# Performance work log

Measured on AMD Instinct MI355X. Metric: run time of the kernel, lower is better.

Reference implementation:

```python
import jax, jax.numpy as jnp
import numpy as np

LUT_DIM = 33  # standard 33^3 color LUT


def setup_inputs() -> dict:
    key = jax.random.key(0)
    k1, k2 = jax.random.split(key)
    # learned 3D LUT: [out_channels=3, D_b, D_g, D_r]
    lut = jax.random.normal(k1, (3, LUT_DIM, LUT_DIM, LUT_DIM), dtype=jnp.float32) * 0.1
    # input image batch in [0, 1): [B, 3, H, W]
    x = jax.random.uniform(k2, (4, 3, 1024, 1024), dtype=jnp.float32)
    return {"lut": lut, "x": x}


def reference(lut, x):
    """Trilinear interpolation of a 3D color LUT (image-adaptive-3DLUT forward).

    lut: [3, D, D, D] laid out as lut[c, ib, ig, ir] (flat index ir + ig*D + ib*D*D)
    x:   [B, 3, H, W] with channels (r, g, b) in [0, 1]
    returns: [B, 3, H, W]
    """
    dim = lut.shape[-1]
    scale = dim - 1  # 1 / binsize

    r, g, b = x[:, 0], x[:, 1], x[:, 2]  # each [B, H, W]

    def cell(c):
        s = c * scale
        idx = jnp.clip(jnp.floor(s), 0, scale - 1).astype(jnp.int32)
        return idx, s - idx.astype(s.dtype)  # integer cell, fractional offset

    ir, dr = cell(r)
    ig, dg = cell(g)
    ib, db = cell(b)

    lut_flat = lut.reshape(3, -1)  # [3, D^3], tiny and cache-resident

    out = jnp.zeros((3,) + r.shape, dtype=x.dtype)  # [3, B, H, W]
    # 8 corners of the enclosing LUT cell, trilinear weights
    for or_ in (0, 1):
        wr = dr if or_ else (1.0 - dr)
        for og in (0, 1):
            wg = dg if og else (1.0 - dg)
            for ob in (0, 1):
                wb = db if ob else (1.0 - db)
                flat = ((ib + ob) * dim + (ig + og)) * dim + (ir + or_)  # [B, H, W]
                corner = lut_flat[:, flat]  # gather -> [3, B, H, W]
                out = out + (wr * wg * wb)[None] * corner

    return jnp.transpose(out, (1, 0, 2, 3))  # [B, 3, H, W]
```

## Files before the change

### kernel.cpp

```cpp
#include <hip/hip_runtime.h>
#include <hip/hip_fp16.h>


#define LUT_D     33
#define LUT_DD    (LUT_D * LUT_D)
#define LUT_N     (LUT_D * LUT_D * LUT_D)
#define CH_STRIDE 35940
#define STAGE_G   (CH_STRIDE / 4)
#define HW4       (1024 * 1024 / 4)
#define NGROUPS   (4 * HW4)
#define THREADS   1024
#define GRID      256
#define GPB       (3 * NGROUPS / GRID)
#define STEPS     6

typedef float vfloat4 __attribute__((ext_vector_type(4)));

__device__ __forceinline__ unsigned int pack2(float a, float b) {
    union { __half2 h; unsigned int u; } cv;
    cv.h = __floats2half2_rn(a, b);
    return cv.u;
}
__device__ __forceinline__ float2 unpack2(unsigned int p) {
    union { unsigned int u; __half2 h; } cv;
    cv.u = p;
    return __half22float2(cv.h);
}

__global__ __launch_bounds__(256)
void lut_pack_kernel(const float* __restrict__ lut, unsigned int* __restrict__ W) {
    const int t = blockIdx.x * 256 + (int)threadIdx.x;
    if (t >= 3 * LUT_N) return;
    const int c = t / LUT_N;
    const int i = t - c * LUT_N;
    const float a = lut[t];
    const float b = (i + LUT_DD < LUT_N) ? lut[t + LUT_DD] : 0.0f;
    W[c * CH_STRIDE + i] = pack2(a, b);
}

__global__ __launch_bounds__(THREADS)
void lut3d_trilerp_kernel(const unsigned int* __restrict__ Wsrc,
                          const float* __restrict__ x,
                          float* __restrict__ out) {
    extern __shared__ __align__(16) unsigned int W[];

    const int t    = (int)threadIdx.x;
    const int base = (int)blockIdx.x * GPB;

    const float4* x4 = (const float4*)x;
    float4*       o4 = (float4*)out;

    auto stage = [&](int c) {
#pragma unroll
        for (int s = 0; s < 9; ++s) {
            const int gid = s * THREADS + t;
            if (gid < STAGE_G) {
                __builtin_amdgcn_global_load_lds(
                    (const __attribute__((address_space(1))) void*)(Wsrc + c * CH_STRIDE + gid * 4),
                    (__attribute__((address_space(3))) void*)(W + gid * 4),
                    16, 0, 0);
            }
        }
    };

    float4 xR[2][2], xG[2][2], xB[2][2];
    int    ibs[2][2];

    auto loadg = [&](int s, int m, int p) {
        const int gg  = base + s * 2048 + m * 1024 + t;
        const int g   = gg & (NGROUPS - 1);
        const int bi  = g >> 18;
        const int hw4 = g & (HW4 - 1);
        const int ib  = bi * 3 * HW4 + hw4;
        ibs[p][m] = ib;
        xR[p][m] = x4[ib];
        xG[p][m] = x4[ib + HW4];
        xB[p][m] = x4[ib + 2 * HW4];
    };

    auto dog = [&](int m, int p, int ch) {
        const float4 R = xR[p][m], G = xG[p][m], B = xB[p][m];
        const float rr[4] = {R.x, R.y, R.z, R.w};
        const float gw[4] = {G.x, G.y, G.z, G.w};
        const float bw[4] = {B.x, B.y, B.z, B.w};

        int   idx[4];
        float dr[4], dg[4], db[4];
#pragma unroll
        for (int k = 0; k < 4; ++k) {
            const float sr = rr[k] * 32.0f;
            const float sg = gw[k] * 32.0f;
            const float sb = bw[k] * 32.0f;
            const float fr = fminf(fmaxf(floorf(sr), 0.0f), 31.0f);
            const float fg = fminf(fmaxf(floorf(sg), 0.0f), 31.0f);
            const float fb = fminf(fmaxf(floorf(sb), 0.0f), 31.0f);
            dr[k] = sr - fr;
            dg[k] = sg - fg;
            db[k] = sb - fb;
            idx[k] = ((int)fb * LUT_D + (int)fg) * LUT_D + (int)fr;
        }

        unsigned int q00[4], q01[4], q10[4], q11[4];
#pragma unroll
        for (int k = 0; k < 4; ++k) {
            q00[k] = W[idx[k]];
            q01[k] = W[idx[k] + 1];
            q10[k] = W[idx[k] + LUT_D];
            q11[k] = W[idx[k] + LUT_D + 1];
        }

        float oo[4];
#pragma unroll
        for (int k = 0; k < 4; ++k) {
            const float2 a = unpack2(q00[k]);
            const float2 b = unpack2(q01[k]);
            const float2 c = unpack2(q10[k]);
            const float2 d = unpack2(q11[k]);
            const float v00 = a.x + db[k] * (a.y - a.x);
            const float v01 = b.x + db[k] * (b.y - b.x);
            const float v10 = c.x + db[k] * (c.y - c.x);
            const float v11 = d.x + db[k] * (d.y - d.x);
            const float v0  = v00 + dr[k] * (v01 - v00);
            const float v1  = v10 + dr[k] * (v11 - v10);
            oo[k] = v0 + dg[k] * (v1 - v0);
        }
        vfloat4 v = {oo[0], oo[1], oo[2], oo[3]};
        __builtin_nontemporal_store(v, (vfloat4*)&o4[ibs[p][m] + ch * HW4]);
    };

    int cur = base >> 20;
    stage(cur);
    loadg(0, 0, 0);
    loadg(0, 1, 0);
    __syncthreads();

#pragma unroll
    for (int s = 0; s < STEPS; ++s) {
        const int p  = s & 1;
        const int pn = p ^ 1;
        const int ch = (base + s * 2048) >> 20;
        if (ch != cur) {
            __syncthreads();
            stage(ch);
            __syncthreads();
            cur = ch;
        }
        if (s + 1 < STEPS) {
            loadg(s + 1, 0, pn);
            loadg(s + 1, 1, pn);
        }
        dog(0, p, ch);
        dog(1, p, ch);
    }
}

extern "C" void kernel_launch(void* const* d_in, const int* in_sizes, int n_in,
                              void* d_out, int out_size, void* d_ws, size_t ws_size,
                              hipStream_t stream) {
    const float*  lut = (const float*)d_in[0];
    const float*  x   = (const float*)d_in[1];
    float*        out = (float*)d_out;
    unsigned int* W   = (unsigned int*)d_ws;

    const int pack_grid = (3 * LUT_N + 255) / 256;
    lut_pack_kernel<<<pack_grid, 256, 0, stream>>>(lut, W);

    const size_t lds_bytes = (size_t)CH_STRIDE * 4;
    lut3d_trilerp_kernel<<<GRID, THREADS, lds_bytes, stream>>>(W, x, out);
}
```

Before: 118.7 us.

## Process all output channels per pixel chunk, caching indices and weights in registers

The grid now splits the pixel groups across blocks, so each block reads each pixel's input only once. The block computes channel 0 and keeps the cell indices and fp16-packed fractional weights in registers. It then restages the LUT in shared memory for channels 1 and 2 and reuses the cached values. This removes the 3x re-read of the input and the repeated index math. The cost is more registers, two extra shared-memory restages per block, and lower weight precision on channels 1 and 2, since the fractions are stored as fp16.

```diff
diff --git a/kernel.cpp b/kernel.cpp
--- a/kernel.cpp
+++ b/kernel.cpp
@@ -9,10 +9,9 @@
 #define STAGE_G   (CH_STRIDE / 4)
 #define HW4       (1024 * 1024 / 4)
 #define NGROUPS   (4 * HW4)
+#define NCHUNKS   256
 #define THREADS   1024
-#define GRID      256
-#define GPB       (3 * NGROUPS / GRID)
-#define STEPS     6
+#define ITERS     (NGROUPS / NCHUNKS / THREADS)
 
 typedef float vfloat4 __attribute__((ext_vector_type(4)));
 
@@ -44,8 +43,8 @@
                           float* __restrict__ out) {
     extern __shared__ __align__(16) unsigned int W[];
 
-    const int t    = (int)threadIdx.x;
-    const int base = (int)blockIdx.x * GPB;
+    const int t  = (int)threadIdx.x;
+    const int g0 = (int)blockIdx.x * (NGROUPS / NCHUNKS) + t;
 
     const float4* x4 = (const float4*)x;
     float4*       o4 = (float4*)out;
@@ -63,29 +62,64 @@
         }
     };
 
-    float4 xR[2][2], xG[2][2], xB[2][2];
-    int    ibs[2][2];
-
-    auto loadg = [&](int s, int m, int p) {
-        const int gg  = base + s * 2048 + m * 1024 + t;
-        const int g   = gg & (NGROUPS - 1);
-        const int bi  = g >> 18;
-        const int hw4 = g & (HW4 - 1);
-        const int ib  = bi * 3 * HW4 + hw4;
-        ibs[p][m] = ib;
-        xR[p][m] = x4[ib];
-        xG[p][m] = x4[ib + HW4];
-        xB[p][m] = x4[ib + 2 * HW4];
+    auto quad = [&](const int idx[4], const float dr4[4], const float dg4[4],
+                    const float db4[4], int obase) {
+        unsigned int q00[4], q01[4], q10[4], q11[4];
+#pragma unroll
+        for (int k = 0; k < 4; ++k) {
+            q00[k] = W[idx[k]];
+            q01[k] = W[idx[k] + 1];
+            q10[k] = W[idx[k] + LUT_D];
+            q11[k] = W[idx[k] + LUT_D + 1];
+        }
+        float oo[4];
+#pragma unroll
+        for (int k = 0; k < 4; ++k) {
+            const float2 a = unpack2(q00[k]);
+            const float2 b = unpack2(q01[k]);
+            const float2 c = unpack2(q10[k]);
+            const float2 d = unpack2(q11[k]);
+            const float v00 = a.x + db4[k] * (a.y - a.x);
+            const float v01 = b.x + db4[k] * (b.y - b.x);
+            const float v10 = c.x + db4[k] * (c.y - c.x);
+            const float v11 = d.x + db4[k] * (d.y - d.x);
+            const float v0  = v00 + dr4[k] * (v01 - v00);
+            const float v1  = v10 + dr4[k] * (v11 - v10);
+            oo[k] = v0 + dg4[k] * (v1 - v0);
+        }
+        vfloat4 v = {oo[0], oo[1], oo[2], oo[3]};
+        __builtin_nontemporal_store(v, (vfloat4*)&o4[obase]);
     };
 
-    auto dog = [&](int m, int p, int ch) {
-        const float4 R = xR[p][m], G = xG[p][m], B = xB[p][m];
-        const float rr[4] = {R.x, R.y, R.z, R.w};
-        const float gw[4] = {G.x, G.y, G.z, G.w};
-        const float bw[4] = {B.x, B.y, B.z, B.w};
+    stage(0);
+    int    ibs[ITERS];
+    float4 R[ITERS], G[ITERS], B[ITERS];
+    {
+        const int bi = g0 >> 18, hw4 = g0 & (HW4 - 1);
+        ibs[0] = bi * 3 * HW4 + hw4;
+        R[0] = x4[ibs[0]];
+        G[0] = x4[ibs[0] + HW4];
+        B[0] = x4[ibs[0] + 2 * HW4];
+    }
+    __syncthreads();
 
-        int   idx[4];
-        float dr[4], dg[4], db[4];
+    unsigned int pidx[ITERS][2], pdr[ITERS][2], pdg[ITERS][2], pdb[ITERS][2];
+
+#pragma unroll
+    for (int it = 0; it < ITERS; ++it) {
+        if (it + 1 < ITERS) {
+            const int g  = g0 + (it + 1) * THREADS;
+            const int bi = g >> 18, hw4 = g & (HW4 - 1);
+            ibs[it + 1] = bi * 3 * HW4 + hw4;
+            R[it + 1] = x4[ibs[it + 1]];
+            G[it + 1] = x4[ibs[it + 1] + HW4];
+            B[it + 1] = x4[ibs[it + 1] + 2 * HW4];
+        }
+        const float rr[4] = {R[it].x, R[it].y, R[it].z, R[it].w};
+        const float gw[4] = {G[it].x, G[it].y, G[it].z, G[it].w};
+        const float bw[4] = {B[it].x, B[it].y, B[it].z, B[it].w};
+
+        int idx[4]; float dr4[4], dg4[4], db4[4];
 #pragma unroll
         for (int k = 0; k < 4; ++k) {
             const float sr = rr[k] * 32.0f;
@@ -94,63 +128,38 @@
             const float fr = fminf(fmaxf(floorf(sr), 0.0f), 31.0f);
             const float fg = fminf(fmaxf(floorf(sg), 0.0f), 31.0f);
             const float fb = fminf(fmaxf(floorf(sb), 0.0f), 31.0f);
-            dr[k] = sr - fr;
-            dg[k] = sg - fg;
-            db[k] = sb - fb;
+            dr4[k] = sr - fr;
+            dg4[k] = sg - fg;
+            db4[k] = sb - fb;
             idx[k] = ((int)fb * LUT_D + (int)fg) * LUT_D + (int)fr;
         }
+        pidx[it][0] = (unsigned)idx[0] | ((unsigned)idx[1] << 16);
+        pidx[it][1] = (unsigned)idx[2] | ((unsigned)idx[3] << 16);
+        pdr[it][0] = pack2(dr4[0], dr4[1]);  pdr[it][1] = pack2(dr4[2], dr4[3]);
+        pdg[it][0] = pack2(dg4[0], dg4[1]);  pdg[it][1] = pack2(dg4[2], dg4[3]);
+        pdb[it][0] = pack2(db4[0], db4[1]);  pdb[it][1] = pack2(db4[2], db4[3]);
 
-        unsigned int q00[4], q01[4], q10[4], q11[4];
-#pragma unroll
-        for (int k = 0; k < 4; ++k) {
-            q00[k] = W[idx[k]];
-            q01[k] = W[idx[k] + 1];
-            q10[k] = W[idx[k] + LUT_D];
-            q11[k] = W[idx[k] + LUT_D + 1];
-        }
-
-        float oo[4];
-#pragma unroll
-        for (int k = 0; k < 4; ++k) {
-            const float2 a = unpack2(q00[k]);
-            const float2 b = unpack2(q01[k]);
-            const float2 c = unpack2(q10[k]);
-            const float2 d = unpack2(q11[k]);
-            const float v00 = a.x + db[k] * (a.y - a.x);
-            const float v01 = b.x + db[k] * (b.y - b.x);
-            const float v10 = c.x + db[k] * (c.y - c.x);
-            const float v11 = d.x + db[k] * (d.y - d.x);
-            const float v0  = v00 + dr[k] * (v01 - v00);
-            const float v1  = v10 + dr[k] * (v11 - v10);
-            oo[k] = v0 + dg[k] * (v1 - v0);
-        }
-        vfloat4 v = {oo[0], oo[1], oo[2], oo[3]};
-        __builtin_nontemporal_store(v, (vfloat4*)&o4[ibs[p][m] + ch * HW4]);
-    };
-
-    int cur = base >> 20;
-    stage(cur);
-    loadg(0, 0, 0);
-    loadg(0, 1, 0);
-    __syncthreads();
+        quad(idx, dr4, dg4, db4, ibs[it]);
+    }
 
 #pragma unroll
-    for (int s = 0; s < STEPS; ++s) {
-        const int p  = s & 1;
-        const int pn = p ^ 1;
-        const int ch = (base + s * 2048) >> 20;
-        if (ch != cur) {
-            __syncthreads();
-            stage(ch);
-            __syncthreads();
-            cur = ch;
+    for (int c = 1; c < 3; ++c) {
+        __syncthreads();
+        stage(c);
+        __syncthreads();
+
+#pragma unroll
+        for (int it = 0; it < ITERS; ++it) {
+            const int idx[4] = {(int)(pidx[it][0] & 0xffffu), (int)(pidx[it][0] >> 16),
+                                (int)(pidx[it][1] & 0xffffu), (int)(pidx[it][1] >> 16)};
+            const float2 r0 = unpack2(pdr[it][0]), r1 = unpack2(pdr[it][1]);
+            const float2 gg = unpack2(pdg[it][0]), g1 = unpack2(pdg[it][1]);
+            const float2 b0 = unpack2(pdb[it][0]), b1 = unpack2(pdb[it][1]);
+            const float dr4[4] = {r0.x, r0.y, r1.x, r1.y};
+            const float dg4[4] = {gg.x, gg.y, g1.x, g1.y};
+            const float db4[4] = {b0.x, b0.y, b1.x, b1.y};
+            quad(idx, dr4, dg4, db4, ibs[it] + c * HW4);
         }
-        if (s + 1 < STEPS) {
-            loadg(s + 1, 0, pn);
-            loadg(s + 1, 1, pn);
-        }
-        dog(0, p, ch);
-        dog(1, p, ch);
     }
 }
 
@@ -166,5 +175,5 @@
     lut_pack_kernel<<<pack_grid, 256, 0, stream>>>(lut, W);
 
     const size_t lds_bytes = (size_t)CH_STRIDE * 4;
-    lut3d_trilerp_kernel<<<GRID, THREADS, lds_bytes, stream>>>(W, x, out);
+    lut3d_trilerp_kernel<<<NCHUNKS, THREADS, lds_bytes, stream>>>(W, x, out);
 }
```

Result: no change. 117.0 us (-1.4%).
